# Performance work log

Hardware: AMD Instinct MI355X
Metric: run time of the kernel (lower is better)

The kernel has to match this reference:

```python
import jax, jax.numpy as jnp
import numpy as np

B, E, NV = 2, 400000, 50000
DE, DV, DC, DOUT = 64, 64, 32, 64
DIN = DE + 2 * DV + DC  # 224


def setup_inputs() -> dict:
    key = jax.random.key(0)
    ks = jax.random.split(key, 7)
    edata = jax.random.normal(ks[0], (B, E, DE), dtype=jnp.float32)
    vdata = jax.random.normal(ks[1], (B, NV, DV), dtype=jnp.float32)
    cdata = jax.random.normal(ks[2], (B, DC), dtype=jnp.float32)
    sender_ids = jax.random.randint(ks[3], (B, E), 0, NV, dtype=jnp.int64)
    receiver_ids = jax.random.randint(ks[4], (B, E), 0, NV, dtype=jnp.int64)
    W = jax.random.normal(ks[5], (DIN, DOUT), dtype=jnp.float32) * (1.0 / np.sqrt(DIN))
    b = jnp.zeros((DOUT,), dtype=jnp.float32)
    return {"edata": edata, "vdata": vdata, "cdata": cdata,
            "sender_ids": sender_ids, "receiver_ids": receiver_ids,
            "W": W, "b": b}


def reference(edata, vdata, cdata, sender_ids, receiver_ids, W, b):
    # gather sender/receiver vertex features: [B,E,DV]
    sender_data = jnp.take_along_axis(vdata, sender_ids[..., None], axis=1)
    receiver_data = jnp.take_along_axis(vdata, receiver_ids[..., None], axis=1)
    # broadcast context per edge: [B,E,DC]
    curr_cdata = jnp.broadcast_to(cdata[:, None, :], (cdata.shape[0], edata.shape[1], cdata.shape[1]))
    # concat along feature dim -> [B,E,DIN], then per-edge-type MLP updater
    etin = jnp.concatenate((edata, sender_data, receiver_data, curr_cdata), axis=2)
    etout = jax.nn.relu(jnp.einsum("bei,io->beo", etin, W) + b)
    return etout
```

## Files before the change

### kernel.cpp

```cpp
#include <hip/hip_runtime.h>
#include <hip/hip_bf16.h>

typedef __bf16 bf16x8 __attribute__((ext_vector_type(8)));
typedef float  f32x4  __attribute__((ext_vector_type(4)));

#define DE_   64
#define DV_   64
#define DC_   32
#define DOUT_ 64
#define DIN_  224
#define NFRAG 28

__global__ void prep_w_kernel(const float* __restrict__ W, __bf16* __restrict__ wf) {
    int f    = blockIdx.x;
    int lane = threadIdx.x;
    int ks = f >> 2, nt = f & 3;
    int col = nt * 16 + (lane & 15);
    int k0  = ks * 32 + (lane >> 4) * 8;
    bf16x8 v;
#pragma unroll
    for (int j = 0; j < 8; ++j)
        v[j] = (__bf16)W[(k0 + j) * DOUT_ + col];
    reinterpret_cast<bf16x8*>(wf)[f * 64 + lane] = v;
}

__global__ void prep_v_kernel(const float* __restrict__ vdata,
                              __bf16* __restrict__ vb16, int n8) {
    int i = blockIdx.x * blockDim.x + threadIdx.x;
    if (i >= n8) return;
    f32x4 a = reinterpret_cast<const f32x4*>(vdata)[2 * i];
    f32x4 b = reinterpret_cast<const f32x4*>(vdata)[2 * i + 1];
    bf16x8 v;
    v[0] = (__bf16)a[0]; v[1] = (__bf16)a[1]; v[2] = (__bf16)a[2]; v[3] = (__bf16)a[3];
    v[4] = (__bf16)b[0]; v[5] = (__bf16)b[1]; v[6] = (__bf16)b[2]; v[7] = (__bf16)b[3];
    reinterpret_cast<bf16x8*>(vb16)[i] = v;
}

__global__ __launch_bounds__(1024, 2)
void edge_mlp_kernel(const float* __restrict__ edata,
                     const __bf16* __restrict__ vb16,
                     const float* __restrict__ cdata,
                     const int*   __restrict__ snd,
                     const int*   __restrict__ rcv,
                     const __bf16* __restrict__ wf,
                     const float* __restrict__ bias,
                     float* __restrict__ out,
                     int NV, int n_tiles, int tiles_per_batch) {
    __shared__ bf16x8 wlds[NFRAG * 64];

    const int tid  = threadIdx.x;
    const int lane = tid & 63;
    const int tile = blockIdx.x * (blockDim.x >> 6) + (tid >> 6);
    const bool active = tile < n_tiles;

    const int lr = lane & 15;
    const int lg = lane >> 4;
    const int kl = lg * 8;

    const int  b   = (tile >= tiles_per_batch) ? 1 : 0;
    const long row = active ? ((long)tile * 16 + lr) : 0;

    const int s = __builtin_nontemporal_load(&snd[row]);
    const int r = __builtin_nontemporal_load(&rcv[row]);

    f32x4 f0[3], f1[3];
#pragma unroll
    for (int ks = 0; ks < 2; ++ks) {
        const f32x4* p = reinterpret_cast<const f32x4*>(edata + row * DE_ + ks * 32 + kl);
        f0[ks] = __builtin_nontemporal_load(p);
        f1[ks] = __builtin_nontemporal_load(p + 1);
    }
    {
        const f32x4* p = reinterpret_cast<const f32x4*>(cdata + b * DC_ + kl);
        f0[2] = p[0];
        f1[2] = p[1];
    }
    float bias_v[4];
#pragma unroll
    for (int nt = 0; nt < 4; ++nt) bias_v[nt] = bias[nt * 16 + lr];

    {
        const bf16x8* wsrc = reinterpret_cast<const bf16x8*>(wf);
        for (int i = tid; i < NFRAG * 64; i += 1024)
            wlds[i] = wsrc[i];
    }
    __syncthreads();

    const __bf16* vbb = vb16 + (long)b * NV * DV_;
    bf16x8 afrag[7];
#pragma unroll
    for (int ks = 2; ks < 6; ++ks) {
        const __bf16* p = (ks < 4) ? (vbb + (long)s * DV_ + (ks - 2) * 32 + kl)
                                   : (vbb + (long)r * DV_ + (ks - 4) * 32 + kl);
        afrag[ks] = *reinterpret_cast<const bf16x8*>(p);
    }
#pragma unroll
    for (int q = 0; q < 3; ++q) {
        int ks = (q < 2) ? q : 6;
        bf16x8 a;
        a[0] = (__bf16)f0[q][0]; a[1] = (__bf16)f0[q][1];
        a[2] = (__bf16)f0[q][2]; a[3] = (__bf16)f0[q][3];
        a[4] = (__bf16)f1[q][0]; a[5] = (__bf16)f1[q][1];
        a[6] = (__bf16)f1[q][2]; a[7] = (__bf16)f1[q][3];
        afrag[ks] = a;
    }

    f32x4 acc[4];
#pragma unroll
    for (int nt = 0; nt < 4; ++nt) acc[nt] = f32x4{0.f, 0.f, 0.f, 0.f};

#pragma unroll
    for (int ks = 0; ks < 7; ++ks) {
#pragma unroll
        for (int nt = 0; nt < 4; ++nt) {
            bf16x8 w = wlds[(ks * 4 + nt) * 64 + lane];
            acc[nt] = __builtin_amdgcn_mfma_f32_16x16x32_bf16(afrag[ks], w, acc[nt], 0, 0, 0);
        }
    }

    if (!active) return;

    const long rb = (long)tile * 16;
#pragma unroll
    for (int nt = 0; nt < 4; ++nt) {
#pragma unroll
        for (int j = 0; j < 4; ++j) {
            float v = acc[nt][j] + bias_v[nt];
            out[(rb + lg * 4 + j) * DOUT_ + nt * 16 + lr] = v > 0.f ? v : 0.f;
        }
    }
}

extern "C" void kernel_launch(void* const* d_in, const int* in_sizes, int n_in,
                              void* d_out, int out_size, void* d_ws, size_t ws_size,
                              hipStream_t stream) {
    const float* edata = (const float*)d_in[0];
    const float* vdata = (const float*)d_in[1];
    const float* cdata = (const float*)d_in[2];
    const int*   snd   = (const int*)d_in[3];
    const int*   rcv   = (const int*)d_in[4];
    const float* W     = (const float*)d_in[5];
    const float* bias  = (const float*)d_in[6];
    float* out = (float*)d_out;

    const int Etot = in_sizes[3];
    const int Bb   = in_sizes[2] / DC_;
    const int E    = Etot / Bb;
    const int NV   = in_sizes[1] / (Bb * DV_);
    const int n_tiles = (Etot + 15) / 16;
    const int tiles_per_batch = E / 16;
    const int nvdata = in_sizes[1];

    __bf16* wf   = (__bf16*)d_ws;
    __bf16* vb16 = (__bf16*)((char*)d_ws + NFRAG * 64 * 16);

    hipLaunchKernelGGL(prep_w_kernel, dim3(NFRAG), dim3(64), 0, stream, W, wf);
    {
        int n8 = nvdata / 8;
        hipLaunchKernelGGL(prep_v_kernel, dim3((n8 + 255) / 256), dim3(256), 0,
                           stream, vdata, vb16, n8);
    }

    const int waves_per_block = 16;
    const int blocks = (n_tiles + waves_per_block - 1) / waves_per_block;
    hipLaunchKernelGGL(edge_mlp_kernel, dim3(blocks), dim3(1024), 0, stream,
                       edata, vb16, cdata, snd, rcv, wf, bias, out,
                       NV, n_tiles, tiles_per_batch);
}
```

Before: 120.0 us.

## Process four edge tiles per wave, amortizing weight LDS staging and prefetching indices

Each wave now handles four consecutive 16-edge tiles in a loop instead of one, so the per-block weight copy into LDS and the barrier are paid over four times more work, and the grid is four times smaller. The sender/receiver indices for the next tile are loaded early to overlap the index load with the gather. The cost is less parallelism (fewer blocks, fewer waves in flight to hide gather latency) and more serialized memory latency per wave.

```diff
diff --git a/kernel.cpp b/kernel.cpp
--- a/kernel.cpp
+++ b/kernel.cpp
@@ -10,6 +10,7 @@
 #define DOUT_ 64
 #define DIN_  224
 #define NFRAG 28
+#define TPW   4
 
 __global__ void prep_w_kernel(const float* __restrict__ W, __bf16* __restrict__ wf) {
     int f    = blockIdx.x;
@@ -50,83 +51,95 @@
 
     const int tid  = threadIdx.x;
     const int lane = tid & 63;
-    const int tile = blockIdx.x * (blockDim.x >> 6) + (tid >> 6);
-    const bool active = tile < n_tiles;
+    const int wid  = blockIdx.x * (blockDim.x >> 6) + (tid >> 6);
 
     const int lr = lane & 15;
     const int lg = lane >> 4;
     const int kl = lg * 8;
 
-    const int  b   = (tile >= tiles_per_batch) ? 1 : 0;
-    const long row = active ? ((long)tile * 16 + lr) : 0;
-
-    const int s = __builtin_nontemporal_load(&snd[row]);
-    const int r = __builtin_nontemporal_load(&rcv[row]);
-
-    f32x4 f0[3], f1[3];
-#pragma unroll
-    for (int ks = 0; ks < 2; ++ks) {
-        const f32x4* p = reinterpret_cast<const f32x4*>(edata + row * DE_ + ks * 32 + kl);
-        f0[ks] = __builtin_nontemporal_load(p);
-        f1[ks] = __builtin_nontemporal_load(p + 1);
-    }
-    {
-        const f32x4* p = reinterpret_cast<const f32x4*>(cdata + b * DC_ + kl);
-        f0[2] = p[0];
-        f1[2] = p[1];
-    }
-    float bias_v[4];
-#pragma unroll
-    for (int nt = 0; nt < 4; ++nt) bias_v[nt] = bias[nt * 16 + lr];
+    const int tile0 = wid * TPW;
 
     {
         const bf16x8* wsrc = reinterpret_cast<const bf16x8*>(wf);
         for (int i = tid; i < NFRAG * 64; i += 1024)
             wlds[i] = wsrc[i];
     }
+
+    float bias_v[4];
+#pragma unroll
+    for (int nt = 0; nt < 4; ++nt) bias_v[nt] = bias[nt * 16 + lr];
+
     __syncthreads();
 
-    const __bf16* vbb = vb16 + (long)b * NV * DV_;
-    bf16x8 afrag[7];
-#pragma unroll
-    for (int ks = 2; ks < 6; ++ks) {
-        const __bf16* p = (ks < 4) ? (vbb + (long)s * DV_ + (ks - 2) * 32 + kl)
-                                   : (vbb + (long)r * DV_ + (ks - 4) * 32 + kl);
-        afrag[ks] = *reinterpret_cast<const bf16x8*>(p);
-    }
-#pragma unroll
-    for (int q = 0; q < 3; ++q) {
-        int ks = (q < 2) ? q : 6;
-        bf16x8 a;
-        a[0] = (__bf16)f0[q][0]; a[1] = (__bf16)f0[q][1];
-        a[2] = (__bf16)f0[q][2]; a[3] = (__bf16)f0[q][3];
-        a[4] = (__bf16)f1[q][0]; a[5] = (__bf16)f1[q][1];
-        a[6] = (__bf16)f1[q][2]; a[7] = (__bf16)f1[q][3];
-        afrag[ks] = a;
-    }
+    if (tile0 >= n_tiles) return;
 
-    f32x4 acc[4];
-#pragma unroll
-    for (int nt = 0; nt < 4; ++nt) acc[nt] = f32x4{0.f, 0.f, 0.f, 0.f};
+    int s = __builtin_nontemporal_load(&snd[(long)tile0 * 16 + lr]);
+    int r = __builtin_nontemporal_load(&rcv[(long)tile0 * 16 + lr]);
 
 #pragma unroll
-    for (int ks = 0; ks < 7; ++ks) {
+    for (int t = 0; t < TPW; ++t) {
+        const int tile = tile0 + t;
+        if (tile >= n_tiles) break;
+
+        const int  b   = (tile >= tiles_per_batch) ? 1 : 0;
+        const long row = (long)tile * 16 + lr;
+
+        const __bf16* vbb = vb16 + (long)b * NV * DV_;
+        bf16x8 afrag[7];
+        afrag[2] = *reinterpret_cast<const bf16x8*>(vbb + (long)s * DV_ + kl);
+        afrag[3] = *reinterpret_cast<const bf16x8*>(vbb + (long)s * DV_ + 32 + kl);
+        afrag[4] = *reinterpret_cast<const bf16x8*>(vbb + (long)r * DV_ + kl);
+        afrag[5] = *reinterpret_cast<const bf16x8*>(vbb + (long)r * DV_ + 32 + kl);
+
+        if (t + 1 < TPW && tile + 1 < n_tiles) {
+            s = __builtin_nontemporal_load(&snd[row + 16]);
+            r = __builtin_nontemporal_load(&rcv[row + 16]);
+        }
+
+        f32x4 f0[3], f1[3];
+#pragma unroll
+        for (int ks = 0; ks < 2; ++ks) {
+            const f32x4* p = reinterpret_cast<const f32x4*>(edata + row * DE_ + ks * 32 + kl);
+            f0[ks] = __builtin_nontemporal_load(p);
+            f1[ks] = __builtin_nontemporal_load(p + 1);
+        }
+        {
+            const f32x4* p = reinterpret_cast<const f32x4*>(cdata + b * DC_ + kl);
+            f0[2] = p[0];
+            f1[2] = p[1];
+        }
+#pragma unroll
+        for (int q = 0; q < 3; ++q) {
+            int ks = (q < 2) ? q : 6;
+            bf16x8 a;
+            a[0] = (__bf16)f0[q][0]; a[1] = (__bf16)f0[q][1];
+            a[2] = (__bf16)f0[q][2]; a[3] = (__bf16)f0[q][3];
+            a[4] = (__bf16)f1[q][0]; a[5] = (__bf16)f1[q][1];
+            a[6] = (__bf16)f1[q][2]; a[7] = (__bf16)f1[q][3];
+            afrag[ks] = a;
+        }
+
+        f32x4 acc[4];
+#pragma unroll
+        for (int nt = 0; nt < 4; ++nt) acc[nt] = f32x4{0.f, 0.f, 0.f, 0.f};
+
+#pragma unroll
+        for (int ks = 0; ks < 7; ++ks) {
+#pragma unroll
+            for (int nt = 0; nt < 4; ++nt) {
+                bf16x8 w = wlds[(ks * 4 + nt) * 64 + lane];
+                acc[nt] = __builtin_amdgcn_mfma_f32_16x16x32_bf16(afrag[ks], w, acc[nt], 0, 0, 0);
+            }
+        }
+
+        const long rb = (long)tile * 16;
 #pragma unroll
         for (int nt = 0; nt < 4; ++nt) {
-            bf16x8 w = wlds[(ks * 4 + nt) * 64 + lane];
-            acc[nt] = __builtin_amdgcn_mfma_f32_16x16x32_bf16(afrag[ks], w, acc[nt], 0, 0, 0);
-        }
-    }
-
-    if (!active) return;
-
-    const long rb = (long)tile * 16;
 #pragma unroll
-    for (int nt = 0; nt < 4; ++nt) {
-#pragma unroll
-        for (int j = 0; j < 4; ++j) {
-            float v = acc[nt][j] + bias_v[nt];
-            out[(rb + lg * 4 + j) * DOUT_ + nt * 16 + lr] = v > 0.f ? v : 0.f;
+            for (int j = 0; j < 4; ++j) {
+                float v = acc[nt][j] + bias_v[nt];
+                out[(rb + lg * 4 + j) * DOUT_ + nt * 16 + lr] = v > 0.f ? v : 0.f;
+            }
         }
     }
 }
@@ -161,8 +174,8 @@
                            stream, vdata, vb16, n8);
     }
 
-    const int waves_per_block = 16;
-    const int blocks = (n_tiles + waves_per_block - 1) / waves_per_block;
+    const int tiles_per_block = 16 * TPW;
+    const int blocks = (n_tiles + tiles_per_block - 1) / tiles_per_block;
     hipLaunchKernelGGL(edge_mlp_kernel, dim3(blocks), dim3(1024), 0, stream,
                        edata, vb16, cdata, snd, rcv, wf, bias, out,
                        NV, n_tiles, tiles_per_batch);
```

Measured after the change: 147.5 us. +23.0%, slower.
